# Kernel optimization log

Hardware: AMD Instinct MI355X
Metric: run time of the kernel (lower is better)

Reference implementation:

```python
import jax, jax.numpy as jnp
import numpy as np

BAND = 8          # band_width
DS = 0.1          # diag_subtract
DILATIONS = (1, 2, 4)
EPS_NORM = 1e-6
EPS_GAP = 1e-6
EPS_LN = 1e-5


def _conv1d(x, w, b, dil=1):
    # x: (B, C_in, T), w: (C_out, C_in, K) torch-style OIH
    pad = dil * (w.shape[-1] // 2)  # 'same' padding as in torch module
    y = jax.lax.conv_general_dilated(
        x, w, window_strides=(1,), padding=[(pad, pad)],
        rhs_dilation=(dil,), dimension_numbers=("NCH", "OIH", "NCH"))
    return y + b[None, :, None]


def _strip(feat, mask, w, ds):
    # Banded cosine SSM: strip[b, idx, t] = ((xn[b,t].xn[b,t+|k|]) - ds*[k==0] + 1)/2 * m[t]*m[t+|k|]
    # Mathematically identical to full S = xn xn^T (symmetric) followed by
    # extract_diagonal_strip, but computes only the (2w+1)-wide band.
    xm = feat * mask[:, :, None]
    xn = xm / (jnp.linalg.norm(xm, axis=-1, keepdims=True) + EPS_NORM)
    T = xn.shape[1]
    rows = []
    for k in range(-w, w + 1):
        a = abs(k)
        dot = jnp.einsum("btd,btd->bt", xn[:, :T - a] if a else xn, xn[:, a:])
        s = (dot - (ds if k == 0 else 0.0) + 1.0) * 0.5
        s = s * mask[:, :T - a] * mask[:, a:] if a else s * mask * mask
        rows.append(jnp.pad(s, ((0, 0), (0, a))))
    return jnp.stack(rows, axis=1)  # (B, 2w+1, T)


def _encode(strip, mask, w_in, b_in, stages):
    h = jax.nn.relu(_conv1d(strip, w_in, b_in))
    for (wd, bd, wp, bp, d) in stages:
        h = jax.nn.relu(_conv1d(h, wd, bd, d))   # dilated k=3 conv (dropout=eval no-op)
        h = jax.nn.relu(_conv1d(h, wp, bp))      # pointwise k=1 conv
    m = mask[:, None, :]
    return (h * m).sum(-1) / (m.sum(-1) + EPS_GAP)  # masked GAP -> (B, C)


def setup_inputs() -> dict:
    key = jax.random.key(0)
    ks = jax.random.split(key, 32)
    B, T, D, C, NB = 32, 4096, 256, 64, 2 * BAND + 1
    s = 0.02
    n = lambda k, shp: (jax.random.normal(k, shp, jnp.float32) * s)
    inp = {
        "video_feat": jax.random.normal(ks[0], (B, T, D), jnp.float32),
        "audio_feat": jax.random.normal(ks[1], (B, T, D), jnp.float32),
        "video_mask": jnp.ones((B, T), jnp.float32),
        "audio_mask": jnp.ones((B, T), jnp.float32),
        "w_in": n(ks[2], (C, NB, 1)), "b_in": jnp.zeros((C,), jnp.float32),
        "w_d1": n(ks[3], (C, C, 3)), "b_d1": jnp.zeros((C,), jnp.float32),
        "w_p1": n(ks[4], (C, C, 1)), "b_p1": jnp.zeros((C,), jnp.float32),
        "w_d2": n(ks[5], (C, C, 3)), "b_d2": jnp.zeros((C,), jnp.float32),
        "w_p2": n(ks[6], (C, C, 1)), "b_p2": jnp.zeros((C,), jnp.float32),
        "w_d3": n(ks[7], (C, C, 3)), "b_d3": jnp.zeros((C,), jnp.float32),
        "w_p3": n(ks[8], (C, C, 1)), "b_p3": jnp.zeros((C,), jnp.float32),
        "ln_g": jnp.ones((2 * C,), jnp.float32), "ln_b": jnp.zeros((2 * C,), jnp.float32),
        "mha_w1": n(ks[9], (2 * C, C)), "mha_b1": jnp.zeros((C,), jnp.float32),
        "mha_w2": n(ks[10], (C, 1)), "mha_b2": -jnp.ones((1,), jnp.float32),
        "ffn_w1": n(ks[11], (2 * C, C)), "ffn_b1": jnp.zeros((C,), jnp.float32),
        "ffn_w2": n(ks[12], (C, 1)), "ffn_b2": jnp.zeros((1,), jnp.float32),
    }
    return inp


def reference(video_feat, audio_feat, video_mask, audio_mask,
              w_in, b_in, w_d1, b_d1, w_p1, b_p1, w_d2, b_d2, w_p2, b_p2,
              w_d3, b_d3, w_p3, b_p3, ln_g, ln_b,
              mha_w1, mha_b1, mha_w2, mha_b2, ffn_w1, ffn_b1, ffn_w2, ffn_b2):
    stages = [(w_d1, b_d1, w_p1, b_p1, DILATIONS[0]),
              (w_d2, b_d2, w_p2, b_p2, DILATIONS[1]),
              (w_d3, b_d3, w_p3, b_p3, DILATIONS[2])]
    z_a = _encode(_strip(audio_feat, audio_mask, BAND, DS), audio_mask, w_in, b_in, stages)
    z_v = _encode(_strip(video_feat, video_mask, BAND, DS), video_mask, w_in, b_in, stages)
    f = jnp.concatenate([z_a, z_v], axis=-1)  # (B, 2C), audio first as in torch
    mu = f.mean(-1, keepdims=True)
    var = ((f - mu) ** 2).mean(-1, keepdims=True)
    fn = (f - mu) / jnp.sqrt(var + EPS_LN) * ln_g + ln_b
    g_mha = jax.nn.sigmoid(jax.nn.relu(fn @ mha_w1 + mha_b1) @ mha_w2 + mha_b2)
    g_ffn = jnp.tanh(jax.nn.relu(fn @ ffn_w1 + ffn_b1) @ ffn_w2 + ffn_b2)
    return (g_mha[:, :, None], g_ffn[:, :, None])  # (B,1,1) each
```

## Files before the change

### kernel.cpp

```cpp
#include <hip/hip_runtime.h>
#include <math.h>

#define B_ 32
#define T_ 4096
#define D_ 256
#define C_ 64
#define EPSN 1e-6f
#define EPSG 1e-6f
#define EPSL 1e-5f
#define DS_ 0.1f

typedef short bfrag __attribute__((ext_vector_type(8)));
typedef float f32x4 __attribute__((ext_vector_type(4)));
typedef unsigned short ushort4_t __attribute__((ext_vector_type(4)));
typedef unsigned short ushort8_t __attribute__((ext_vector_type(8)));

static __device__ __forceinline__ unsigned short f2bf(float f) {
    unsigned int u = __builtin_bit_cast(unsigned int, f);
    unsigned int r = u + 0x7fffu + ((u >> 16) & 1u);
    return (unsigned short)(r >> 16);
}
static __device__ __forceinline__ float bf2f(unsigned short u) {
    return __builtin_bit_cast(float, ((unsigned int)u) << 16);
}

static __device__ __forceinline__ f32x4 mfma_bf16(bfrag a, bfrag b, f32x4 c) {
    return __builtin_amdgcn_mfma_f32_16x16x32_bf16(a, b, c, 0, 0, 0);
}

__global__ __launch_bounds__(256) void prepack_kernel(
    const float* __restrict__ w_in,
    const float* __restrict__ wd0, const float* __restrict__ wp0,
    const float* __restrict__ wd1, const float* __restrict__ wp1,
    const float* __restrict__ wd2, const float* __restrict__ wp2,
    unsigned short* __restrict__ wk)
{
    int idx = blockIdx.x * 256 + threadIdx.x;
    if (idx >= 1024 + 3 * 16384) return;
    if (idx < 1024) {
        int c = idx >> 4, a = idx & 15;
        float wv = 0.f;
        if (a <= 8) {
            wv = w_in[c * 17 + 8 + a];
            if (a > 0) wv += w_in[c * 17 + 8 - a];
        }
        wk[idx] = f2bf(wv);
    } else {
        int i2 = idx - 1024;
        int s = i2 >> 14;
        int r = i2 & 16383;
        const float* wd = s == 0 ? wd0 : (s == 1 ? wd1 : wd2);
        const float* wp = s == 0 ? wp0 : (s == 1 ? wp1 : wp2);
        unsigned short v;
        if (r < 12288) {
            int c = r / 192, k = r - c * 192;
            int tap = k >> 6, ci = k & 63;
            v = f2bf(wd[c * 192 + ci * 3 + tap]);
        } else {
            v = f2bf(wp[r - 12288]);
        }
        wk[idx] = v;
    }
}

#define RB 64
#define DBP 33

__global__ __launch_bounds__(256, 4) void strip_kernel(
    const float* __restrict__ feat0, const float* __restrict__ mask0,
    const float* __restrict__ feat1, const float* __restrict__ mask1,
    unsigned short* __restrict__ s16g)
{
    __shared__ float dotbuf[4 * 16 * DBP];
    __shared__ float scl[72];
    __shared__ float msk[72];
    __shared__ float sdh[8];

    int bid  = blockIdx.x;
    int tile = bid & 63;
    int b    = (bid >> 6) & 31;
    int mod  = bid >> 11;
    int mb   = mod * B_ + b;
    const float* feat = mod ? feat1 : feat0;
    const float* mask = mod ? mask1 : mask0;
    int t0 = tile * RB;
    int tid = threadIdx.x;
    int w = tid >> 6, lane = tid & 63;
    int l15 = lane & 15, lg = lane >> 4;

    if (tid < 72) {
        int tg = t0 + tid;
        msk[tid] = (tg < T_) ? mask[(size_t)b * T_ + tg] : 0.f;
    }

    {
        int tA = t0 + w * 16 + l15;
        int tB = tA + 16;
        bool okB = (tB < T_);
        const float* baseA = feat + ((size_t)b * T_ + tA) * D_ + lg * 8;
        const float* baseB = feat + ((size_t)b * T_ + (okB ? tB : 0)) * D_ + lg * 8;
        f32x4 acc0 = {0.f, 0.f, 0.f, 0.f}, acc1 = {0.f, 0.f, 0.f, 0.f};
        #pragma unroll
        for (int ks = 0; ks < 8; ++ks) {
            float4 al = *(const float4*)(baseA + ks * 32);
            float4 ah = *(const float4*)(baseA + ks * 32 + 4);
            float4 bl = okB ? *(const float4*)(baseB + ks * 32)     : make_float4(0.f, 0.f, 0.f, 0.f);
            float4 bh = okB ? *(const float4*)(baseB + ks * 32 + 4) : make_float4(0.f, 0.f, 0.f, 0.f);
            bfrag av, bv;
            av[0] = (short)f2bf(al.x); av[1] = (short)f2bf(al.y);
            av[2] = (short)f2bf(al.z); av[3] = (short)f2bf(al.w);
            av[4] = (short)f2bf(ah.x); av[5] = (short)f2bf(ah.y);
            av[6] = (short)f2bf(ah.z); av[7] = (short)f2bf(ah.w);
            bv[0] = (short)f2bf(bl.x); bv[1] = (short)f2bf(bl.y);
            bv[2] = (short)f2bf(bl.z); bv[3] = (short)f2bf(bl.w);
            bv[4] = (short)f2bf(bh.x); bv[5] = (short)f2bf(bh.y);
            bv[6] = (short)f2bf(bh.z); bv[7] = (short)f2bf(bh.w);
            acc0 = mfma_bf16(av, av, acc0);
            acc1 = mfma_bf16(av, bv, acc1);
        }
        #pragma unroll
        for (int r = 0; r < 4; ++r) {
            dotbuf[w * 16 * DBP + (lg * 4 + r) * DBP + l15] = acc0[r];
            dotbuf[w * 16 * DBP + (lg * 4 + r) * DBP + 16 + l15] = acc1[r];
        }
    }

    {
        int l5 = lane & 31;
        int r = 64 + w * 2 + (lane >> 5);
        int tg = t0 + r;
        float ss = 0.f;
        if (tg < T_) {
            const float* p = feat + ((size_t)b * T_ + tg) * D_ + l5 * 8;
            float4 v0 = *(const float4*)(p);
            float4 v1 = *(const float4*)(p + 4);
            float f;
            f = bf2f(f2bf(v0.x)); ss += f * f;
            f = bf2f(f2bf(v0.y)); ss += f * f;
            f = bf2f(f2bf(v0.z)); ss += f * f;
            f = bf2f(f2bf(v0.w)); ss += f * f;
            f = bf2f(f2bf(v1.x)); ss += f * f;
            f = bf2f(f2bf(v1.y)); ss += f * f;
            f = bf2f(f2bf(v1.z)); ss += f * f;
            f = bf2f(f2bf(v1.w)); ss += f * f;
        }
        ss += __shfl_xor(ss, 1);
        ss += __shfl_xor(ss, 2);
        ss += __shfl_xor(ss, 4);
        ss += __shfl_xor(ss, 8);
        ss += __shfl_xor(ss, 16);
        if (l5 == 0) sdh[r - 64] = ss;
    }
    __syncthreads();

    if (tid < 72) {
        float sd = (tid < 64) ? dotbuf[(tid >> 4) * 16 * DBP + (tid & 15) * DBP + (tid & 15)]
                              : sdh[tid - 64];
        float m = msk[tid];
        float nm = m * sqrtf(sd);
        scl[tid] = m / (nm + EPSN);
    }
    __syncthreads();

    if (tid < RB) {
        int t = tid, wq = t >> 4, r = t & 15;
        float m_t = msk[t], sc_t = scl[t];
        ushort8_t o0, o1;
        #pragma unroll
        for (int e = 0; e < 8; ++e) { o0[e] = 0; o1[e] = 0; }
        #pragma unroll
        for (int a = 0; a <= 8; ++a) {
            float dot = dotbuf[wq * 16 * DBP + r * DBP + r + a];
            float dn = dot * sc_t * scl[t + a];
            float s = (dn - (a == 0 ? DS_ : 0.f) + 1.f) * 0.5f * m_t * msk[t + a];
            if (a < 8) o0[a] = f2bf(s); else o1[0] = f2bf(s);
        }
        unsigned short* dst = s16g + ((size_t)mb * T_ + t0 + t) * 16;
        *(ushort8_t*)dst = o0;
        *(ushort8_t*)(dst + 8) = o1;
    }
}

#define TT 128
#define G_ 16
#define WB 160
#define SBP 24
#define OFF_BUFA 8192
#define OFF_BUFB 28672
#define OFF_MLD  49664
#define OFF_RED  50176
#define SMEM_TOT (OFF_RED + 1024)

static __device__ __forceinline__ int swzi(int row, int su, int off) {
    return row * 64 + ((su ^ (row & 7)) << 3) + off;
}

template<int DIL>
static __device__ __forceinline__ void conv_stage(
    const unsigned short* __restrict__ wdg, const unsigned short* __restrict__ wpg,
    unsigned short* __restrict__ bufIn, unsigned short* __restrict__ bufOut,
    const float* __restrict__ b_d, const float* __restrict__ b_p,
    int t0, int l15, int lg, int mt0, int wn)
{
    {
        bfrag ad[2][6];
        float bd[2][4];
        #pragma unroll
        for (int m = 0; m < 2; ++m) {
            int row = (mt0 + m) * 16 + l15;
            #pragma unroll
            for (int ks = 0; ks < 6; ++ks) {
                int tap = ks >> 1, half = ks & 1;
                ad[m][ks] = *(const bfrag*)(wdg + row * 192 + tap * 64 + half * 32 + lg * 8);
            }
            #pragma unroll
            for (int r = 0; r < 4; ++r) bd[m][r] = b_d[(mt0 + m) * 16 + lg * 4 + r];
        }
        for (int nt = wn * 5; nt < wn * 5 + 5; ++nt) {
            int j = nt * 16 + l15;
            f32x4 acc0 = {0.f, 0.f, 0.f, 0.f}, acc1 = {0.f, 0.f, 0.f, 0.f};
            #pragma unroll
            for (int ks = 0; ks < 6; ++ks) {
                int tap = ks >> 1, half = ks & 1;
                int brow = j + (tap - 1) * DIL;
                bfrag bv = *(const bfrag*)(bufIn + swzi(brow, half * 4 + lg, 0));
                acc0 = mfma_bf16(ad[0][ks], bv, acc0);
                acc1 = mfma_bf16(ad[1][ks], bv, acc1);
            }
            int tg = t0 - G_ + j;
            bool valid = (tg >= 0 && tg < T_);
            #pragma unroll
            for (int m = 0; m < 2; ++m) {
                f32x4 acc = m ? acc1 : acc0;
                ushort4_t pk;
                #pragma unroll
                for (int r = 0; r < 4; ++r) {
                    float v = acc[r] + bd[m][r];
                    v = valid ? fmaxf(v, 0.f) : 0.f;
                    pk[r] = f2bf(v);
                }
                *(ushort4_t*)(bufOut + swzi(j, (mt0 + m) * 2 + (lg >> 1), (lg & 1) * 4)) = pk;
            }
        }
    }
    __syncthreads();

    {
        bfrag ap[2][2];
        float bpv[2][4];
        #pragma unroll
        for (int m = 0; m < 2; ++m) {
            int row = (mt0 + m) * 16 + l15;
            #pragma unroll
            for (int half = 0; half < 2; ++half)
                ap[m][half] = *(const bfrag*)(wpg + row * 64 + half * 32 + lg * 8);
            #pragma unroll
            for (int r = 0; r < 4; ++r) bpv[m][r] = b_p[(mt0 + m) * 16 + lg * 4 + r];
        }
        for (int nt = wn * 5; nt < wn * 5 + 5; ++nt) {
            int j = nt * 16 + l15;
            f32x4 acc0 = {0.f, 0.f, 0.f, 0.f}, acc1 = {0.f, 0.f, 0.f, 0.f};
            #pragma unroll
            for (int half = 0; half < 2; ++half) {
                bfrag bv = *(const bfrag*)(bufOut + swzi(j, half * 4 + lg, 0));
                acc0 = mfma_bf16(ap[0][half], bv, acc0);
                acc1 = mfma_bf16(ap[1][half], bv, acc1);
            }
            int tg = t0 - G_ + j;
            bool valid = (tg >= 0 && tg < T_);
            #pragma unroll
            for (int m = 0; m < 2; ++m) {
                f32x4 acc = m ? acc1 : acc0;
                ushort4_t pk;
                #pragma unroll
                for (int r = 0; r < 4; ++r) {
                    float v = acc[r] + bpv[m][r];
                    v = valid ? fmaxf(v, 0.f) : 0.f;
                    pk[r] = f2bf(v);
                }
                *(ushort4_t*)(bufIn + swzi(j, (mt0 + m) * 2 + (lg >> 1), (lg & 1) * 4)) = pk;
            }
        }
    }
    __syncthreads();
}

__global__ __launch_bounds__(256, 3) void conv_mfma_kernel(
    const unsigned short* __restrict__ s16g,
    const float* __restrict__ mask0, const float* __restrict__ mask1,
    const unsigned short* __restrict__ wk,
    const float* __restrict__ b_in,
    const float* __restrict__ b_d1, const float* __restrict__ b_p1,
    const float* __restrict__ b_d2, const float* __restrict__ b_p2,
    const float* __restrict__ b_d3, const float* __restrict__ b_p3,
    float* __restrict__ z_part)
{
    __shared__ __align__(16) char smem[SMEM_TOT];
    unsigned short* sbuf = (unsigned short*)smem;
    unsigned short* bufA = (unsigned short*)(smem + OFF_BUFA);
    unsigned short* bufB = (unsigned short*)(smem + OFF_BUFB);
    float* mld = (float*)(smem + OFF_MLD);
    float* red = (float*)(smem + OFF_RED);

    int bid  = blockIdx.x;
    int tile = bid & 31;
    int b    = (bid >> 5) & 31;
    int mod  = bid >> 10;
    int mb   = mod * B_ + b;
    const float* mask = mod ? mask1 : mask0;
    int t0  = tile * TT;
    int tid = threadIdx.x;
    int lane = tid & 63;
    int w = tid >> 6;
    int l15 = lane & 15, lg = lane >> 4;
    int wm = w >> 1, wn = w & 1;
    int mt0 = wm * 2;

    const unsigned short* weff_g = wk;

    {
        const unsigned short* srow = s16g + (size_t)mb * T_ * 16;
        for (int ch = tid; ch < WB * 2; ch += 256) {
            int j = ch >> 1, q = ch & 1;
            int t = t0 - G_ + j;
            ushort8_t v = {0, 0, 0, 0, 0, 0, 0, 0};
            if (t >= 0 && t < T_) v = *(const ushort8_t*)(srow + (size_t)t * 16 + q * 8);
            *(ushort8_t*)(sbuf + j * SBP + q * 8) = v;
        }
        if (tid < TT) {
            int tg = t0 + tid;
            mld[tid] = (tg < T_) ? mask[(size_t)b * T_ + tg] : 0.f;
        }
    }
    __syncthreads();

    {
        int lg2 = lg & 1;
        bfrag a_in[2];
        float bi[2][4];
        #pragma unroll
        for (int m = 0; m < 2; ++m) {
            int row = (mt0 + m) * 16 + l15;
            a_in[m] = *(const bfrag*)(weff_g + row * 16 + lg2 * 8);
            #pragma unroll
            for (int r = 0; r < 4; ++r) bi[m][r] = b_in[(mt0 + m) * 16 + lg * 4 + r];
        }
        for (int nt = wn * 5; nt < wn * 5 + 5; ++nt) {
            int j = nt * 16 + l15;
            bfrag bv = {0, 0, 0, 0, 0, 0, 0, 0};
            if (lg < 2) bv = *(const bfrag*)(sbuf + j * SBP + lg * 8);
            f32x4 acc0 = {0.f, 0.f, 0.f, 0.f}, acc1 = {0.f, 0.f, 0.f, 0.f};
            acc0 = mfma_bf16(a_in[0], bv, acc0);
            acc1 = mfma_bf16(a_in[1], bv, acc1);
            int tg = t0 - G_ + j;
            bool valid = (tg >= 0 && tg < T_);
            #pragma unroll
            for (int m = 0; m < 2; ++m) {
                f32x4 acc = m ? acc1 : acc0;
                ushort4_t pk;
                #pragma unroll
                for (int r = 0; r < 4; ++r) {
                    float v = acc[r] + bi[m][r];
                    v = valid ? fmaxf(v, 0.f) : 0.f;
                    pk[r] = f2bf(v);
                }
                *(ushort4_t*)(bufA + swzi(j, (mt0 + m) * 2 + (lg >> 1), (lg & 1) * 4)) = pk;
            }
        }
    }
    __syncthreads();

    conv_stage<1>(wk + 1024,             wk + 1024 + 12288,             bufA, bufB, b_d1, b_p1, t0, l15, lg, mt0, wn);
    conv_stage<2>(wk + 1024 + 16384,     wk + 1024 + 16384 + 12288,     bufA, bufB, b_d2, b_p2, t0, l15, lg, mt0, wn);
    conv_stage<4>(wk + 1024 + 2 * 16384, wk + 1024 + 2 * 16384 + 12288, bufA, bufB, b_d3, b_p3, t0, l15, lg, mt0, wn);

    {
        int c = tid & 63, g = tid >> 6;
        float acc = 0.f;
        #pragma unroll 4
        for (int i = 0; i < 32; ++i) {
            int jj = g * 32 + i;
            int r = G_ + jj;
            acc += bf2f(bufA[swzi(r, c >> 3, c & 7)]) * mld[jj];
        }
        red[g * 64 + c] = acc;
    }
    __syncthreads();
    if (tid < 64) {
        float z = red[tid] + red[64 + tid] + red[128 + tid] + red[192 + tid];
        z_part[((size_t)mb * 32 + tile) * 64 + tid] = z;
    }
}

__global__ __launch_bounds__(128) void gates_kernel(
    const float* __restrict__ z_part,
    const float* __restrict__ mask0, const float* __restrict__ mask1,
    const float* __restrict__ ln_g, const float* __restrict__ ln_b,
    const float* __restrict__ mha_w1, const float* __restrict__ mha_b1,
    const float* __restrict__ mha_w2, const float* __restrict__ mha_b2,
    const float* __restrict__ ffn_w1, const float* __restrict__ ffn_b1,
    const float* __restrict__ ffn_w2, const float* __restrict__ ffn_b2,
    float* __restrict__ out)
{
    __shared__ float fn[128];
    __shared__ float red[4];
    __shared__ float msum[2];
    int b = blockIdx.x, tid = threadIdx.x;
    int mod = tid >> 6, c = tid & 63;

    float z = 0.f;
    for (int tl = 0; tl < 32; ++tl)
        z += z_part[((size_t)(mod * B_ + b) * 32 + tl) * 64 + c];

    const float* mk = mod ? mask1 : mask0;
    float ms = 0.f;
    for (int t = c; t < T_; t += 64) ms += mk[(size_t)b * T_ + t];
    #pragma unroll
    for (int o = 32; o > 0; o >>= 1) ms += __shfl_xor(ms, o);
    if (c == 0) msum[mod] = ms;
    __syncthreads();

    float fv = z / (msum[mod] + EPSG);
    float s1 = fv, s2 = fv * fv;
    #pragma unroll
    for (int o = 32; o > 0; o >>= 1) { s1 += __shfl_xor(s1, o); s2 += __shfl_xor(s2, o); }
    if (c == 0) { red[mod * 2] = s1; red[mod * 2 + 1] = s2; }
    __syncthreads();

    float mu  = (red[0] + red[2]) * (1.0f / 128.0f);
    float ex2 = (red[1] + red[3]) * (1.0f / 128.0f);
    float var = ex2 - mu * mu;
    float fnv = (fv - mu) * rsqrtf(var + EPSL) * ln_g[tid] + ln_b[tid];
    fn[tid] = fnv;
    __syncthreads();

    const float* W1 = mod ? ffn_w1 : mha_w1;
    const float* B1 = mod ? ffn_b1 : mha_b1;
    const float* W2 = mod ? ffn_w2 : mha_w2;
    const float* B2 = mod ? ffn_b2 : mha_b2;
    float r = B1[c];
    for (int i = 0; i < 128; ++i) r += fn[i] * W1[i * 64 + c];
    r = fmaxf(r, 0.f);
    float g = r * W2[c];
    #pragma unroll
    for (int o = 32; o > 0; o >>= 1) g += __shfl_xor(g, o);
    if (c == 0) {
        g += B2[0];
        out[mod * B_ + b] = mod ? tanhf(g) : 1.0f / (1.0f + expf(-g));
    }
}

extern "C" void kernel_launch(void* const* d_in, const int* in_sizes, int n_in,
                              void* d_out, int out_size, void* d_ws, size_t ws_size,
                              hipStream_t stream) {
    const float* video_feat = (const float*)d_in[0];
    const float* audio_feat = (const float*)d_in[1];
    const float* video_mask = (const float*)d_in[2];
    const float* audio_mask = (const float*)d_in[3];
    const float* w_in = (const float*)d_in[4];
    const float* b_in = (const float*)d_in[5];
    const float* w_d1 = (const float*)d_in[6];
    const float* b_d1 = (const float*)d_in[7];
    const float* w_p1 = (const float*)d_in[8];
    const float* b_p1 = (const float*)d_in[9];
    const float* w_d2 = (const float*)d_in[10];
    const float* b_d2 = (const float*)d_in[11];
    const float* w_p2 = (const float*)d_in[12];
    const float* b_p2 = (const float*)d_in[13];
    const float* w_d3 = (const float*)d_in[14];
    const float* b_d3 = (const float*)d_in[15];
    const float* w_p3 = (const float*)d_in[16];
    const float* b_p3 = (const float*)d_in[17];
    const float* ln_g = (const float*)d_in[18];
    const float* ln_b = (const float*)d_in[19];
    const float* mha_w1 = (const float*)d_in[20];
    const float* mha_b1 = (const float*)d_in[21];
    const float* mha_w2 = (const float*)d_in[22];
    const float* mha_b2 = (const float*)d_in[23];
    const float* ffn_w1 = (const float*)d_in[24];
    const float* ffn_b1 = (const float*)d_in[25];
    const float* ffn_w2 = (const float*)d_in[26];
    const float* ffn_b2 = (const float*)d_in[27];

    unsigned short* s16g = (unsigned short*)d_ws;
    float* z_part = (float*)((char*)d_ws + (size_t)2 * B_ * T_ * 16 * 2);
    unsigned short* wk = (unsigned short*)((char*)z_part + (size_t)2 * B_ * 32 * 64 * 4);

    prepack_kernel<<<dim3(196), dim3(256), 0, stream>>>(
        w_in, w_d1, w_p1, w_d2, w_p2, w_d3, w_p3, wk);

    strip_kernel<<<dim3(2 * B_ * (T_ / RB)), dim3(256), 0, stream>>>(
        audio_feat, audio_mask, video_feat, video_mask, s16g);

    conv_mfma_kernel<<<dim3(2 * B_ * (T_ / TT)), dim3(256), 0, stream>>>(
        s16g, audio_mask, video_mask, wk, b_in,
        b_d1, b_p1, b_d2, b_p2, b_d3, b_p3, z_part);

    gates_kernel<<<dim3(B_), dim3(128), 0, stream>>>(
        z_part, audio_mask, video_mask, ln_g, ln_b,
        mha_w1, mha_b1, mha_w2, mha_b2, ffn_w1, ffn_b1, ffn_w2, ffn_b2,
        (float*)d_out);
}
```

Measured before the change: 163.3 us.

## Stage strip-kernel feature tiles into LDS via async double-buffered global_load_lds

Replaces direct per-thread global float4 loads in the strip kernel with async global-to-LDS loads of 64-float column chunks, double-buffered across four chunks of D, with an XOR swizzle to avoid bank conflicts. Each row is loaded once into LDS and reused for the A, B and halo norm computations instead of being reloaded from global. The block index is also remapped to change scheduling order. LDS use grows (about 40KB per block), so occupancy hint drops from 4 to 3 blocks per CU, and manual waitcnt/barrier sequencing adds correctness risk.

```diff
diff --git a/kernel.cpp b/kernel.cpp
--- a/kernel.cpp
+++ b/kernel.cpp
@@ -26,6 +26,12 @@
 
 static __device__ __forceinline__ f32x4 mfma_bf16(bfrag a, bfrag b, f32x4 c) {
     return __builtin_amdgcn_mfma_f32_16x16x32_bf16(a, b, c, 0, 0, 0);
+}
+
+static __device__ __forceinline__ void gload_lds16(const float* g, float* l) {
+    __builtin_amdgcn_global_load_lds(
+        (const __attribute__((address_space(1))) unsigned int*)(g),
+        (__attribute__((address_space(3))) unsigned int*)(l), 16, 0, 0);
 }
 
 __global__ __launch_bounds__(256) void prepack_kernel(
@@ -65,18 +71,23 @@
 
 #define RB 64
 #define DBP 33
-
-__global__ __launch_bounds__(256, 4) void strip_kernel(
+#define CHUNKF 64
+#define XROWS 80
+#define XBUF_F (XROWS * CHUNKF)
+
+__global__ __launch_bounds__(256, 3) void strip_kernel(
     const float* __restrict__ feat0, const float* __restrict__ mask0,
     const float* __restrict__ feat1, const float* __restrict__ mask1,
     unsigned short* __restrict__ s16g)
 {
+    __shared__ float xbuf[2 * XBUF_F];
     __shared__ float dotbuf[4 * 16 * DBP];
-    __shared__ float scl[72];
-    __shared__ float msk[72];
+    __shared__ float scl[80];
+    __shared__ float msk[80];
     __shared__ float sdh[8];
 
-    int bid  = blockIdx.x;
+    int bid0 = blockIdx.x;
+    int bid  = (bid0 & 7) * 512 + (bid0 >> 3);
     int tile = bid & 63;
     int b    = (bid >> 6) & 31;
     int mod  = bid >> 11;
@@ -88,69 +99,108 @@
     int w = tid >> 6, lane = tid & 63;
     int l15 = lane & 15, lg = lane >> 4;
 
-    if (tid < 72) {
+    if (tid < 80) {
         int tg = t0 + tid;
         msk[tid] = (tg < T_) ? mask[(size_t)b * T_ + tg] : 0.f;
     }
 
-    {
-        int tA = t0 + w * 16 + l15;
-        int tB = tA + 16;
-        bool okB = (tB < T_);
-        const float* baseA = feat + ((size_t)b * T_ + tA) * D_ + lg * 8;
-        const float* baseB = feat + ((size_t)b * T_ + (okB ? tB : 0)) * D_ + lg * 8;
-        f32x4 acc0 = {0.f, 0.f, 0.f, 0.f}, acc1 = {0.f, 0.f, 0.f, 0.f};
-        #pragma unroll
-        for (int ks = 0; ks < 8; ++ks) {
-            float4 al = *(const float4*)(baseA + ks * 32);
-            float4 ah = *(const float4*)(baseA + ks * 32 + 4);
-            float4 bl = okB ? *(const float4*)(baseB + ks * 32)     : make_float4(0.f, 0.f, 0.f, 0.f);
-            float4 bh = okB ? *(const float4*)(baseB + ks * 32 + 4) : make_float4(0.f, 0.f, 0.f, 0.f);
+    const float* fb = feat + (size_t)b * T_ * D_;
+
+    auto stage_chunk = [&](int ct, int bf) {
+        #pragma unroll
+        for (int i = 0; i < 5; ++i) {
+            int gi = w * 5 + i;
+            int row = gi * 4 + (lane >> 4);
+            int tg = t0 + row; if (tg >= T_) tg = 0;
+            const float* gp = fb + (size_t)tg * D_ + ct * CHUNKF
+                              + (((lane & 15) ^ (row & 7)) << 2);
+            gload_lds16(gp, xbuf + bf * XBUF_F + gi * 256);
+        }
+    };
+
+    int rA = w * 16 + l15;
+    int rB = rA + 16;
+    int a7 = rA & 7, b7 = rB & 7;
+    int rh = 64 + w * 2 + (lane >> 5);
+    int l5 = lane & 31;
+    int gh = l5 >> 1, he = (l5 & 1) * 2, h7 = rh & 7;
+
+    f32x4 acc0 = {0.f, 0.f, 0.f, 0.f}, acc1 = {0.f, 0.f, 0.f, 0.f};
+    float acc_h = 0.f;
+
+    auto compute_chunk = [&](const float* xb) {
+        const float* pa = xb + rA * 64;
+        const float* pb = xb + rB * 64;
+        #pragma unroll
+        for (int q = 0; q < 2; ++q) {
+            int g0 = q * 8 + lg * 2;
+            float4 a0 = *(const float4*)(pa + ((g0 ^ a7) << 2));
+            float4 a1 = *(const float4*)(pa + (((g0 + 1) ^ a7) << 2));
+            float4 b0 = *(const float4*)(pb + ((g0 ^ b7) << 2));
+            float4 b1 = *(const float4*)(pb + (((g0 + 1) ^ b7) << 2));
             bfrag av, bv;
-            av[0] = (short)f2bf(al.x); av[1] = (short)f2bf(al.y);
-            av[2] = (short)f2bf(al.z); av[3] = (short)f2bf(al.w);
-            av[4] = (short)f2bf(ah.x); av[5] = (short)f2bf(ah.y);
-            av[6] = (short)f2bf(ah.z); av[7] = (short)f2bf(ah.w);
-            bv[0] = (short)f2bf(bl.x); bv[1] = (short)f2bf(bl.y);
-            bv[2] = (short)f2bf(bl.z); bv[3] = (short)f2bf(bl.w);
-            bv[4] = (short)f2bf(bh.x); bv[5] = (short)f2bf(bh.y);
-            bv[6] = (short)f2bf(bh.z); bv[7] = (short)f2bf(bh.w);
+            av[0] = (short)f2bf(a0.x); av[1] = (short)f2bf(a0.y);
+            av[2] = (short)f2bf(a0.z); av[3] = (short)f2bf(a0.w);
+            av[4] = (short)f2bf(a1.x); av[5] = (short)f2bf(a1.y);
+            av[6] = (short)f2bf(a1.z); av[7] = (short)f2bf(a1.w);
+            bv[0] = (short)f2bf(b0.x); bv[1] = (short)f2bf(b0.y);
+            bv[2] = (short)f2bf(b0.z); bv[3] = (short)f2bf(b0.w);
+            bv[4] = (short)f2bf(b1.x); bv[5] = (short)f2bf(b1.y);
+            bv[6] = (short)f2bf(b1.z); bv[7] = (short)f2bf(b1.w);
             acc0 = mfma_bf16(av, av, acc0);
             acc1 = mfma_bf16(av, bv, acc1);
         }
-        #pragma unroll
-        for (int r = 0; r < 4; ++r) {
-            dotbuf[w * 16 * DBP + (lg * 4 + r) * DBP + l15] = acc0[r];
-            dotbuf[w * 16 * DBP + (lg * 4 + r) * DBP + 16 + l15] = acc1[r];
-        }
-    }
-
-    {
-        int l5 = lane & 31;
-        int r = 64 + w * 2 + (lane >> 5);
-        int tg = t0 + r;
-        float ss = 0.f;
-        if (tg < T_) {
-            const float* p = feat + ((size_t)b * T_ + tg) * D_ + l5 * 8;
-            float4 v0 = *(const float4*)(p);
-            float4 v1 = *(const float4*)(p + 4);
-            float f;
-            f = bf2f(f2bf(v0.x)); ss += f * f;
-            f = bf2f(f2bf(v0.y)); ss += f * f;
-            f = bf2f(f2bf(v0.z)); ss += f * f;
-            f = bf2f(f2bf(v0.w)); ss += f * f;
-            f = bf2f(f2bf(v1.x)); ss += f * f;
-            f = bf2f(f2bf(v1.y)); ss += f * f;
-            f = bf2f(f2bf(v1.z)); ss += f * f;
-            f = bf2f(f2bf(v1.w)); ss += f * f;
-        }
-        ss += __shfl_xor(ss, 1);
-        ss += __shfl_xor(ss, 2);
-        ss += __shfl_xor(ss, 4);
-        ss += __shfl_xor(ss, 8);
-        ss += __shfl_xor(ss, 16);
-        if (l5 == 0) sdh[r - 64] = ss;
-    }
+        const float* hp = xb + rh * 64 + ((gh ^ h7) << 2) + he;
+        float h0 = bf2f(f2bf(hp[0]));
+        float h1 = bf2f(f2bf(hp[1]));
+        acc_h += h0 * h0 + h1 * h1;
+    };
+
+    stage_chunk(0, 0);
+    stage_chunk(1, 1);
+
+    asm volatile("s_waitcnt vmcnt(5)" ::: "memory");
+    __builtin_amdgcn_sched_barrier(0);
+    __builtin_amdgcn_s_barrier();
+    compute_chunk(xbuf);
+    asm volatile("s_waitcnt lgkmcnt(0)" ::: "memory");
+    __builtin_amdgcn_sched_barrier(0);
+    __builtin_amdgcn_s_barrier();
+    stage_chunk(2, 0);
+
+    asm volatile("s_waitcnt vmcnt(5)" ::: "memory");
+    __builtin_amdgcn_sched_barrier(0);
+    __builtin_amdgcn_s_barrier();
+    compute_chunk(xbuf + XBUF_F);
+    asm volatile("s_waitcnt lgkmcnt(0)" ::: "memory");
+    __builtin_amdgcn_sched_barrier(0);
+    __builtin_amdgcn_s_barrier();
+    stage_chunk(3, 1);
+
+    asm volatile("s_waitcnt vmcnt(5)" ::: "memory");
+    __builtin_amdgcn_sched_barrier(0);
+    __builtin_amdgcn_s_barrier();
+    compute_chunk(xbuf);
+    asm volatile("s_waitcnt lgkmcnt(0)" ::: "memory");
+    __builtin_amdgcn_sched_barrier(0);
+    __builtin_amdgcn_s_barrier();
+
+    asm volatile("s_waitcnt vmcnt(0)" ::: "memory");
+    __builtin_amdgcn_sched_barrier(0);
+    __builtin_amdgcn_s_barrier();
+    compute_chunk(xbuf + XBUF_F);
+
+    #pragma unroll
+    for (int r = 0; r < 4; ++r) {
+        dotbuf[w * 16 * DBP + (lg * 4 + r) * DBP + l15] = acc0[r];
+        dotbuf[w * 16 * DBP + (lg * 4 + r) * DBP + 16 + l15] = acc1[r];
+    }
+    acc_h += __shfl_xor(acc_h, 1);
+    acc_h += __shfl_xor(acc_h, 2);
+    acc_h += __shfl_xor(acc_h, 4);
+    acc_h += __shfl_xor(acc_h, 8);
+    acc_h += __shfl_xor(acc_h, 16);
+    if (l5 == 0) sdh[rh - 64] = acc_h;
     __syncthreads();
 
     if (tid < 72) {
```

After: 143.9 us. 1.14x faster.
